# Kernel optimization log

Hardware: AMD Instinct MI355X
Metric: run time of the kernel (lower is better)

Reference implementation:

```python
import jax, jax.numpy as jnp
import numpy as np

SEQ_LEN = 1024
D_MODEL = 512
K_FILT = 24
HEADS = 8
R = 512  # must equal d_model for the module's forward to type-check
NFFT = 2048  # nearest power of two >= 2*SEQ_LEN-1
LN_EPS = 1e-5


def _spectral_filters():
    # Hankel matrix Z[i,j] = 2 / ((i+j)^3 - (i+j)), i,j in 1..T
    e = np.arange(1, SEQ_LEN + 1, dtype=np.float64)
    ipj = e[:, None] + e[None, :]
    Z = 2.0 / (ipj ** 3 - ipj)
    sigma, phi = np.linalg.eigh(Z)
    sigma_k = np.clip(sigma[-K_FILT:], 1e-9, None)
    phi_k = phi[:, -K_FILT:] * sigma_k ** 0.25
    return phi_k.astype(np.float32)  # (T, K)


def setup_inputs() -> dict:
    key = jax.random.key(0)
    ks = jax.random.split(key, 12)
    s = 0.02
    B = 2

    def lin(k):
        kw, kb = jax.random.split(k)
        return (jax.random.normal(kw, (D_MODEL, D_MODEL), jnp.float32) * s,
                jax.random.normal(kb, (D_MODEL,), jnp.float32) * s)

    Wq, bq = lin(ks[0]); Wk, bk = lin(ks[1]); Wv, bv = lin(ks[2])
    Wg, bg = lin(ks[3]); Wo, bo = lin(ks[4])
    return {
        'x': jax.random.normal(ks[5], (B, SEQ_LEN, D_MODEL), jnp.float32),
        'stu_filters': jnp.asarray(_spectral_filters()),
        'M_inputs': jax.random.normal(ks[6], (D_MODEL, R), jnp.float32) * s,
        'M_filters': jax.random.normal(ks[7], (K_FILT, R), jnp.float32) * s,
        'Wq': Wq, 'bq': bq, 'Wk': Wk, 'bk': bk, 'Wv': Wv, 'bv': bv,
        'Wg': Wg, 'bg': bg, 'Wo': Wo, 'bo': bo,
        'ln_w': jnp.ones((R,), jnp.float32),
        'ln_b': jnp.zeros((R,), jnp.float32),
    }


def _stu_conv(u, v):
    # u: (B, T, r), v: (T, r). FFT-based causal conv with sign featurization.
    T = u.shape[1]
    sgn = jnp.where(jnp.arange(T) % 2 == 1, -1.0, 1.0)[None, :, None]  # (1,T,1)
    Vf = jnp.fft.rfft(v[None, :, :, None], n=NFFT, axis=1)  # (1,F,r,1)
    U = jnp.stack([u, u * sgn], axis=-1)  # (B,T,r,2)
    Uf = jnp.fft.rfft(U, n=NFFT, axis=1)  # (B,F,r,2)
    conv = jnp.fft.irfft(Vf * Uf, n=NFFT, axis=1)[:, :T]  # (B,T,r,2)
    return conv[..., 0], conv[..., 1] * sgn


def _layernorm(x, w, b):
    mu = jnp.mean(x, axis=-1, keepdims=True)
    var = jnp.mean((x - mu) ** 2, axis=-1, keepdims=True)
    return (x - mu) * jax.lax.rsqrt(var + LN_EPS) * w + b


def reference(x, stu_filters, M_inputs, M_filters, Wq, bq, Wk, bk, Wv, bv,
              Wg, bg, Wo, bo, ln_w, ln_b):
    B, T, d = x.shape
    hd = d // HEADS
    # STU features
    u_proj = x @ M_inputs                    # (B,T,r)
    phi_proj = stu_filters @ M_filters       # (T,r)
    sp, sm = _stu_conv(u_proj, phi_proj)
    x_tilde = _layernorm(sp + sm, ln_w, ln_b)  # (B,T,r==d)
    # gated linear attention with gelu features and causal cumsum state
    def proj(W, b):
        y = (x @ W.T + b).reshape(B, T, HEADS, hd).transpose(0, 2, 1, 3)
        return jax.nn.gelu(y, approximate=True)
    Q = proj(Wq, bq); K = proj(Wk, bk); V = proj(Wv, bv)
    Zt = jnp.einsum('bhtp,bhtn->bhtpn', V, K)   # (B,H,T,hd,hd)
    Hc = jnp.cumsum(Zt, axis=2)
    Y = jnp.einsum('bhtp,bhtpn->bhtn', Q, Hc)   # (B,H,T,hd)
    Y_attn = Y.transpose(0, 2, 1, 3).reshape(B, T, d)
    gate = jax.nn.sigmoid(x @ Wg.T + bg)
    comb = gate * Y_attn + (1.0 - gate) * x_tilde
    return comb @ Wo.T + bo
```

## Files before the change

### kernel.cpp

```cpp
#include <hip/hip_runtime.h>
#include <hip/hip_bf16.h>

#define T_SEQ 1024
#define D_MOD 512
#define NHEAD 8
#define HDIM  64
#define R_DIM 512
#define BATCH 2

typedef __attribute__((ext_vector_type(8))) __bf16 bf16x8;
typedef __attribute__((ext_vector_type(4))) float f32x4;

__device__ __forceinline__ float ldin(const void* p, size_t i, int bf) {
    if (bf) return __bfloat162float(((const __hip_bfloat16*)p)[i]);
    return ((const float*)p)[i];
}
__device__ __forceinline__ void stout(void* p, size_t i, int bf, float v) {
    if (bf) ((__hip_bfloat16*)p)[i] = __float2bfloat16(v);
    else    ((float*)p)[i] = v;
}

__device__ __forceinline__ float gelu_f(float x) {
    return 0.5f * x * (1.f + tanhf(0.7978845608028654f * (x + 0.044715f * x * x * x)));
}

__device__ __forceinline__ int detect_bf(const void* x) {
    __shared__ int cnt;
    if (threadIdx.x == 0) cnt = 0;
    __syncthreads();
    const unsigned short* h = (const unsigned short*)x;
    int c = 0;
    for (int i = threadIdx.x; i < 8192; i += 256)
        if ((h[i] & 0x7F80u) == 0x7F80u) c++;
    if (c) atomicAdd(&cnt, c);
    __syncthreads();
    return cnt == 0;
}

__global__ __launch_bounds__(256) void mega_gemm(
    const void* __restrict__ x, const void* __restrict__ Mi,
    const void* __restrict__ stf, const void* __restrict__ Mf,
    const void* __restrict__ Wq, const void* __restrict__ bq,
    const void* __restrict__ Wk, const void* __restrict__ bk,
    const void* __restrict__ Wv, const void* __restrict__ bv,
    const void* __restrict__ Wg, const void* __restrict__ bg,
    float* __restrict__ fu, float* __restrict__ fphi,
    __bf16* __restrict__ fQ, __bf16* __restrict__ fKT,
    __bf16* __restrict__ fV, __bf16* __restrict__ fG)
{
    const int tid = threadIdx.x;
    const int job = blockIdx.z;
    if (job == 6) {
        float4* zp = (float4*)fu;
        zp = (float4*)(fphi + 524288);
        const int bid = blockIdx.y * 8 + blockIdx.x;
        const float4 z4 = make_float4(0.f, 0.f, 0.f, 0.f);
        #pragma unroll
        for (int q = 0; q < 8; ++q)
            zp[bid * 2048 + q * 256 + tid] = z4;
        return;
    }
    const int bf = detect_bf(x);
    const void* A = x; const void* Bw; const void* bias = nullptr;
    int Kd = 512, act = 0; bool trb = true;
    switch (job) {
        case 0: Bw = Mi; trb = false; break;
        case 1: Bw = Wq; bias = bq; act = 1; break;
        case 2: Bw = Wk; bias = bk; act = 1; break;
        case 3: Bw = Wv; bias = bv; act = 1; break;
        case 4: Bw = Wg; bias = bg; act = 2; break;
        default: A = stf; Bw = Mf; trb = false; Kd = 32; break;
    }
    const int M = (job == 5) ? 1024 : 2048;
    const int m0 = blockIdx.y * 64;
    if (m0 >= M) return;
    const int n0 = blockIdx.x * 64;

    __shared__ __align__(16) __bf16 As[64][40];
    __shared__ __align__(16) __bf16 Bs[64][40];
    const int wave = tid >> 6, lane = tid & 63;
    const int lm = lane & 15, kq = lane >> 4;

    f32x4 acc[4] = {{0.f,0.f,0.f,0.f},{0.f,0.f,0.f,0.f},
                    {0.f,0.f,0.f,0.f},{0.f,0.f,0.f,0.f}};

    for (int k0 = 0; k0 < Kd; k0 += 32) {
        if (k0) __syncthreads();
        {
            const int mo = tid >> 2;
            const int ko = (tid & 3) * 8;
            if (job == 5) {
                #pragma unroll
                for (int q = 0; q < 8; ++q) {
                    const int k = ko + q;
                    As[mo][k] = (k < 24) ? (__bf16)ldin(A, (size_t)(m0 + mo) * 24 + k, bf)
                                         : (__bf16)0.f;
                }
            } else {
                const size_t off = (size_t)(m0 + mo) * 512 + k0 + ko;
                if (bf) {
                    *(bf16x8*)&As[mo][ko] = *(const bf16x8*)((const __bf16*)A + off);
                } else {
                    const float* Af = (const float*)A + off;
                    const float4 f0 = *(const float4*)Af;
                    const float4 f1 = *(const float4*)(Af + 4);
                    bf16x8 t;
                    t[0]=(__bf16)f0.x; t[1]=(__bf16)f0.y; t[2]=(__bf16)f0.z; t[3]=(__bf16)f0.w;
                    t[4]=(__bf16)f1.x; t[5]=(__bf16)f1.y; t[6]=(__bf16)f1.z; t[7]=(__bf16)f1.w;
                    *(bf16x8*)&As[mo][ko] = t;
                }
            }
        }
        if (trb) {
            const int no = tid >> 2;
            const int ko = (tid & 3) * 8;
            const size_t off = (size_t)(n0 + no) * 512 + k0 + ko;
            if (bf) {
                *(bf16x8*)&Bs[no][ko] = *(const bf16x8*)((const __bf16*)Bw + off);
            } else {
                const float* Bf = (const float*)Bw + off;
                const float4 f0 = *(const float4*)Bf;
                const float4 f1 = *(const float4*)(Bf + 4);
                bf16x8 t;
                t[0]=(__bf16)f0.x; t[1]=(__bf16)f0.y; t[2]=(__bf16)f0.z; t[3]=(__bf16)f0.w;
                t[4]=(__bf16)f1.x; t[5]=(__bf16)f1.y; t[6]=(__bf16)f1.z; t[7]=(__bf16)f1.w;
                *(bf16x8*)&Bs[no][ko] = t;
            }
        } else {
            const int kk = tid >> 3;
            const int nn = (tid & 7) * 8;
            if (job == 5) {
                #pragma unroll
                for (int q = 0; q < 8; ++q)
                    Bs[nn + q][kk] = (kk < 24) ? (__bf16)ldin(Bw, (size_t)kk * 512 + n0 + nn + q, bf)
                                               : (__bf16)0.f;
            } else {
                const size_t off = (size_t)(k0 + kk) * 512 + n0 + nn;
                if (bf) {
                    const bf16x8 t = *(const bf16x8*)((const __bf16*)Bw + off);
                    #pragma unroll
                    for (int q = 0; q < 8; ++q) Bs[nn + q][kk] = t[q];
                } else {
                    const float* Bf = (const float*)Bw + off;
                    #pragma unroll
                    for (int q = 0; q < 8; ++q) Bs[nn + q][kk] = (__bf16)Bf[q];
                }
            }
        }
        __syncthreads();
        const bf16x8 a = *(const bf16x8*)&As[wave * 16 + lm][kq * 8];
        #pragma unroll
        for (int nt = 0; nt < 4; ++nt) {
            const bf16x8 b = *(const bf16x8*)&Bs[nt * 16 + lm][kq * 8];
            acc[nt] = __builtin_amdgcn_mfma_f32_16x16x32_bf16(a, b, acc[nt], 0, 0, 0);
        }
    }
    #pragma unroll
    for (int nt = 0; nt < 4; ++nt) {
        const int n = n0 + nt * 16 + lm;
        #pragma unroll
        for (int r2 = 0; r2 < 4; ++r2) {
            const int m = m0 + wave * 16 + kq * 4 + r2;
            float v = acc[nt][r2];
            if (bias) v += ldin(bias, (size_t)n, bf);
            if (act == 1) v = gelu_f(v);
            if (act == 2) v = 1.f / (1.f + expf(-v));
            switch (job) {
                case 0: fu[(size_t)m * 512 + n] = v; break;
                case 5: fphi[(size_t)m * 512 + n] = v; break;
                case 1: fQ[(size_t)m * 512 + n] = (__bf16)v; break;
                case 3: fV[(size_t)m * 512 + n] = (__bf16)v; break;
                case 4: fG[(size_t)m * 512 + n] = (__bf16)v; break;
                case 2: {
                    const int b = m >> 10, t = m & 1023;
                    const int h = n >> 6,  p = n & 63;
                    fKT[(((size_t)b * NHEAD + h) * 64 + p) * T_SEQ + t] = (__bf16)v;
                    break;
                }
            }
        }
    }
}

__global__ __launch_bounds__(256) void conv_attn_k(
    const float* __restrict__ u, const float* __restrict__ vphi,
    float* __restrict__ w,
    const __bf16* __restrict__ Q, const __bf16* __restrict__ KT,
    const __bf16* __restrict__ V, float* __restrict__ Y)
{
    __shared__ __align__(16) unsigned char smem[49152];
    const int tid = threadIdx.x;
    const int z = blockIdx.z;
    int rem = blockIdx.x, ti = 0;
    while (rem >= ((ti + 4) >> 2)) { rem -= (ti + 4) >> 2; ++ti; }
    const int jlo = rem * 4;
    const int jhi = (jlo + 3 < ti) ? jlo + 3 : ti;
    const int t0 = ti * 64;

    if (z < 2) {
        float (*vs)[64] = (float (*)[64])smem;
        float (*us)[64] = (float (*)[64])(smem + 16384);
        const int rl = tid & 63, tg = tid >> 6;
        const int b = z;
        const int r0 = blockIdx.y * 64;
        const float* ub = u + (size_t)b * T_SEQ * R_DIM;
        float acc[16] = {};
        for (int j = jlo; j <= jhi; ++j) {
            if (j != jlo) __syncthreads();
            const int L0 = j * 64;
            const int W0 = t0 - L0 - 63;
            #pragma unroll
            for (int jj = 0; jj < 8; ++jj) {
                const int n = jj * 256 + tid;
                const int row = n >> 4, c4 = (n & 15) * 4;
                int s = W0 + row;
                s = s < 0 ? 0 : (s > T_SEQ - 1 ? T_SEQ - 1 : s);
                *(float4*)&us[row][c4] = *(const float4*)&ub[(size_t)s * R_DIM + r0 + c4];
            }
            #pragma unroll
            for (int jj = 0; jj < 4; ++jj) {
                const int n = jj * 256 + tid;
                const int row = n >> 4, c4 = (n & 15) * 4;
                *(float4*)&vs[row][c4] = *(const float4*)&vphi[(size_t)(L0 + row) * R_DIM + r0 + c4];
            }
            __syncthreads();
            if (j < ti) {
                #pragma unroll
                for (int g = 0; g < 4; ++g) {
                    const int wsmin = tg * 16 + 49 - 16 * g;
                    float ur[30];
                    #pragma unroll
                    for (int q = 0; q < 30; ++q) ur[q] = us[wsmin + q][rl];
                    float vr[8];
                    #pragma unroll
                    for (int e = 0; e < 8; ++e) vr[e] = vs[16 * g + 2 * e][rl];
                    #pragma unroll
                    for (int e = 0; e < 8; ++e)
                        #pragma unroll
                        for (int i = 0; i < 16; ++i)
                            acc[i] += vr[e] * ur[i - 2 * e + 14];
                }
            } else {
                for (int l = 0; l < 64; l += 2) {
                    const float vv = vs[l][rl];
                    #pragma unroll
                    for (int i = 0; i < 16; ++i) {
                        const int srel = tg * 16 + i - l;
                        if (srel >= 0) acc[i] += vv * us[srel + 63][rl];
                    }
                }
            }
        }
        #pragma unroll
        for (int i = 0; i < 16; ++i)
            atomicAdd(&w[((size_t)b * T_SEQ + t0 + tg * 16 + i) * R_DIM + r0 + rl],
                      2.f * acc[i]);
    } else {
        __bf16 (*Qs)[72] = (__bf16 (*)[72])smem;
        __bf16 (*Vs)[72] = (__bf16 (*)[72])(smem + 9216);
        __bf16 (*Kt)[72] = (__bf16 (*)[72])(smem + 18432);
        __bf16 (*Sa)[72] = (__bf16 (*)[72])(smem + 27648);
        const int wave = tid >> 6, lane = tid & 63;
        const int lm = lane & 15, kq = lane >> 4;
        const int b = z - 2;
        const int h = blockIdx.y;
        const size_t cbase = ((size_t)b * T_SEQ) * D_MOD + h * HDIM;
        const __bf16* KTh = KT + (((size_t)b * NHEAD + h) * 64) * T_SEQ;
        #pragma unroll
        for (int it = 0; it < 2; ++it) {
            const int n = it * 256 + tid;
            const int row = n >> 3, p0 = (n & 7) * 8;
            *(bf16x8*)&Qs[row][p0] = *(const bf16x8*)&Q[cbase + (size_t)(t0 + row) * D_MOD + p0];
        }
        f32x4 accY[4] = {{0.f,0.f,0.f,0.f},{0.f,0.f,0.f,0.f},
                         {0.f,0.f,0.f,0.f},{0.f,0.f,0.f,0.f}};
        for (int j = jlo; j <= jhi; ++j) {
            const int s0 = j * 64;
            __syncthreads();
            #pragma unroll
            for (int it = 0; it < 2; ++it) {
                const int n = it * 256 + tid;
                const int row = n >> 3, c0 = (n & 7) * 8;
                *(bf16x8*)&Vs[row][c0] = *(const bf16x8*)&V[cbase + (size_t)(s0 + row) * D_MOD + c0];
                *(bf16x8*)&Kt[row][c0] = *(const bf16x8*)&KTh[(size_t)row * T_SEQ + s0 + c0];
            }
            __syncthreads();
            f32x4 sacc[4] = {{0.f,0.f,0.f,0.f},{0.f,0.f,0.f,0.f},
                             {0.f,0.f,0.f,0.f},{0.f,0.f,0.f,0.f}};
            #pragma unroll
            for (int ks = 0; ks < 2; ++ks) {
                const bf16x8 a = *(const bf16x8*)&Qs[wave * 16 + lm][ks * 32 + kq * 8];
                #pragma unroll
                for (int nt = 0; nt < 4; ++nt) {
                    const bf16x8 bb = *(const bf16x8*)&Vs[nt * 16 + lm][ks * 32 + kq * 8];
                    sacc[nt] = __builtin_amdgcn_mfma_f32_16x16x32_bf16(a, bb, sacc[nt], 0, 0, 0);
                }
            }
            const bool diag = (j == ti);
            #pragma unroll
            for (int nt = 0; nt < 4; ++nt) {
                const int sl = nt * 16 + lm;
                #pragma unroll
                for (int r2 = 0; r2 < 4; ++r2) {
                    const int tl = wave * 16 + kq * 4 + r2;
                    float v = sacc[nt][r2];
                    if (diag && sl > tl) v = 0.f;
                    Sa[tl][sl] = (__bf16)v;
                }
            }
            #pragma unroll
            for (int ks = 0; ks < 2; ++ks) {
                const bf16x8 a = *(const bf16x8*)&Sa[wave * 16 + lm][ks * 32 + kq * 8];
                #pragma unroll
                for (int nt = 0; nt < 4; ++nt) {
                    const bf16x8 bb = *(const bf16x8*)&Kt[nt * 16 + lm][ks * 32 + kq * 8];
                    accY[nt] = __builtin_amdgcn_mfma_f32_16x16x32_bf16(a, bb, accY[nt], 0, 0, 0);
                }
            }
        }
        #pragma unroll
        for (int nt = 0; nt < 4; ++nt) {
            const int nh = nt * 16 + lm;
            #pragma unroll
            for (int r2 = 0; r2 < 4; ++r2) {
                const int tl = wave * 16 + kq * 4 + r2;
                atomicAdd(&Y[cbase + (size_t)(t0 + tl) * D_MOD + nh], accY[nt][r2]);
            }
        }
    }
}

__global__ __launch_bounds__(256) void ln_k(float* __restrict__ w,
                                            const void* __restrict__ g,
                                            const void* __restrict__ b,
                                            const void* __restrict__ xref)
{
    const int bf = detect_bf(xref);
    const size_t row = (size_t)blockIdx.y * T_SEQ + blockIdx.x;
    float* p = w + row * R_DIM;
    const int tid = threadIdx.x;
    const float x0 = p[tid], x1 = p[tid + 256];
    __shared__ float red[4];
    float s = x0 + x1;
    #pragma unroll
    for (int off = 32; off > 0; off >>= 1) s += __shfl_down(s, off, 64);
    if ((tid & 63) == 0) red[tid >> 6] = s;
    __syncthreads();
    const float mu = (red[0] + red[1] + red[2] + red[3]) * (1.f / 512.f);
    __syncthreads();
    const float d0 = x0 - mu, d1 = x1 - mu;
    float vsum = d0 * d0 + d1 * d1;
    #pragma unroll
    for (int off = 32; off > 0; off >>= 1) vsum += __shfl_down(vsum, off, 64);
    if ((tid & 63) == 0) red[tid >> 6] = vsum;
    __syncthreads();
    const float var = (red[0] + red[1] + red[2] + red[3]) * (1.f / 512.f);
    const float rs = rsqrtf(var + 1e-5f);
    p[tid]       = d0 * rs * ldin(g, tid, bf)       + ldin(b, tid, bf);
    p[tid + 256] = d1 * rs * ldin(g, tid + 256, bf) + ldin(b, tid + 256, bf);
}

__global__ __launch_bounds__(256) void final_gemm(const __bf16* __restrict__ G,
                                                  const float* __restrict__ Yf,
                                                  const float* __restrict__ Xt,
                                                  const void* __restrict__ Wo,
                                                  const void* __restrict__ bo,
                                                  void* __restrict__ out,
                                                  const void* __restrict__ xref)
{
    const int bf = detect_bf(xref);
    __shared__ __align__(16) __bf16 As[64][40];
    __shared__ __align__(16) __bf16 Bs[64][40];
    const int tid = threadIdx.x;
    const int wave = tid >> 6, lane = tid & 63;
    const int lm = lane & 15, kq = lane >> 4;
    const int m0 = blockIdx.y * 64, n0 = blockIdx.x * 64;

    f32x4 acc[4] = {{0.f,0.f,0.f,0.f},{0.f,0.f,0.f,0.f},
                    {0.f,0.f,0.f,0.f},{0.f,0.f,0.f,0.f}};

    for (int k0 = 0; k0 < 512; k0 += 32) {
        __syncthreads();
        {
            const int mo = tid >> 2;
            const int ko = (tid & 3) * 8;
            const size_t off = (size_t)(m0 + mo) * 512 + k0 + ko;
            const bf16x8 g8 = *(const bf16x8*)(G + off);
            const float4 y0 = *(const float4*)(Yf + off);
            const float4 y1 = *(const float4*)(Yf + off + 4);
            const float4 x0 = *(const float4*)(Xt + off);
            const float4 x1 = *(const float4*)(Xt + off + 4);
            const float yv[8] = {y0.x,y0.y,y0.z,y0.w,y1.x,y1.y,y1.z,y1.w};
            const float xv[8] = {x0.x,x0.y,x0.z,x0.w,x1.x,x1.y,x1.z,x1.w};
            bf16x8 t;
            #pragma unroll
            for (int q = 0; q < 8; ++q) {
                const float gg = (float)g8[q];
                t[q] = (__bf16)(gg * yv[q] + (1.f - gg) * xv[q]);
            }
            *(bf16x8*)&As[mo][ko] = t;
        }
        {
            const int no = tid >> 2;
            const int ko = (tid & 3) * 8;
            const size_t off = (size_t)(n0 + no) * 512 + k0 + ko;
            if (bf) {
                *(bf16x8*)&Bs[no][ko] = *(const bf16x8*)((const __bf16*)Wo + off);
            } else {
                const float* Bf = (const float*)Wo + off;
                const float4 f0 = *(const float4*)Bf;
                const float4 f1 = *(const float4*)(Bf + 4);
                bf16x8 t;
                t[0]=(__bf16)f0.x; t[1]=(__bf16)f0.y; t[2]=(__bf16)f0.z; t[3]=(__bf16)f0.w;
                t[4]=(__bf16)f1.x; t[5]=(__bf16)f1.y; t[6]=(__bf16)f1.z; t[7]=(__bf16)f1.w;
                *(bf16x8*)&Bs[no][ko] = t;
            }
        }
        __syncthreads();
        const bf16x8 a = *(const bf16x8*)&As[wave * 16 + lm][kq * 8];
        #pragma unroll
        for (int nt = 0; nt < 4; ++nt) {
            const bf16x8 b = *(const bf16x8*)&Bs[nt * 16 + lm][kq * 8];
            acc[nt] = __builtin_amdgcn_mfma_f32_16x16x32_bf16(a, b, acc[nt], 0, 0, 0);
        }
    }
    #pragma unroll
    for (int nt = 0; nt < 4; ++nt) {
        const int n = n0 + nt * 16 + lm;
        #pragma unroll
        for (int r2 = 0; r2 < 4; ++r2) {
            const int m = m0 + wave * 16 + kq * 4 + r2;
            float v = acc[nt][r2] + ldin(bo, (size_t)n, bf);
            stout(out, (size_t)m * 512 + n, bf, v);
        }
    }
}

extern "C" void kernel_launch(void* const* d_in, const int* in_sizes, int n_in,
                              void* d_out, int out_size, void* d_ws, size_t ws_size,
                              hipStream_t stream)
{
    const void* x   = d_in[0];
    const void* stf = d_in[1];
    const void* Mi  = d_in[2];
    const void* Mf  = d_in[3];
    const void* Wq  = d_in[4];  const void* bq = d_in[5];
    const void* Wk  = d_in[6];  const void* bk = d_in[7];
    const void* Wv  = d_in[8];  const void* bv = d_in[9];
    const void* Wg  = d_in[10]; const void* bg = d_in[11];
    const void* Wo  = d_in[12]; const void* bo = d_in[13];
    const void* lnw = d_in[14]; const void* lnb = d_in[15];

    float* base = (float*)d_ws;
    float*  f_u   = base;
    float*  f_phi = base + 1048576;
    float*  f_w   = base + 1572864;
    float*  f_Y   = base + 2621440;
    __bf16* f_Q   = (__bf16*)(base + 3670016);
    __bf16* f_KT  = f_Q + 1048576;
    __bf16* f_V   = f_KT + 1048576;
    __bf16* f_G   = f_V + 1048576;

    dim3 blk(256);

    mega_gemm<<<dim3(8, 32, 7), blk, 0, stream>>>(
        x, Mi, stf, Mf, Wq, bq, Wk, bk, Wv, bv, Wg, bg,
        f_u, f_phi, f_Q, f_KT, f_V, f_G);

    conv_attn_k<<<dim3(40, 8, 4), blk, 0, stream>>>(f_u, f_phi, f_w, f_Q, f_KT, f_V, f_Y);

    ln_k<<<dim3(T_SEQ, BATCH), blk, 0, stream>>>(f_w, lnw, lnb, x);

    final_gemm<<<dim3(8, 32), blk, 0, stream>>>(f_G, f_Y, f_w, Wo, bo, d_out, x);
}
```

Before: 193.3 us.

## Enlarge mega_gemm tiles to 128x64 with K=64 steps and LDS-staged K transpose

The projection GEMM kernel now computes 128x64 output tiles per block, with two M-subtiles per wave and a 64-wide K step, which halves the grid and the number of barrier iterations. Weight loads for the non-transposed B path are vectorised into 8-element LDS stores. The transposed K output is staged through shared memory and written with coalesced 16-byte stores instead of strided scalar writes. The zero-fill job is resized to match the smaller grid. The cost is more LDS and registers per block and fewer blocks available to fill the GPU.

```diff
diff --git a/kernel.cpp b/kernel.cpp
--- a/kernel.cpp
+++ b/kernel.cpp
@@ -51,135 +51,162 @@
     const int tid = threadIdx.x;
     const int job = blockIdx.z;
     if (job == 6) {
-        float4* zp = (float4*)fu;
-        zp = (float4*)(fphi + 524288);
+        float4* zp = (float4*)(fphi + 524288);
         const int bid = blockIdx.y * 8 + blockIdx.x;
         const float4 z4 = make_float4(0.f, 0.f, 0.f, 0.f);
         #pragma unroll
-        for (int q = 0; q < 8; ++q)
-            zp[bid * 2048 + q * 256 + tid] = z4;
+        for (int q = 0; q < 16; ++q)
+            zp[(size_t)bid * 4096 + q * 256 + tid] = z4;
         return;
     }
     const int bf = detect_bf(x);
     const void* A = x; const void* Bw; const void* bias = nullptr;
-    int Kd = 512, act = 0; bool trb = true;
+    int act = 0; bool trb = true;
     switch (job) {
         case 0: Bw = Mi; trb = false; break;
         case 1: Bw = Wq; bias = bq; act = 1; break;
         case 2: Bw = Wk; bias = bk; act = 1; break;
         case 3: Bw = Wv; bias = bv; act = 1; break;
         case 4: Bw = Wg; bias = bg; act = 2; break;
-        default: A = stf; Bw = Mf; trb = false; Kd = 32; break;
+        default: A = stf; Bw = Mf; trb = false; break;
     }
     const int M = (job == 5) ? 1024 : 2048;
-    const int m0 = blockIdx.y * 64;
+    const int Kd = (job == 5) ? 64 : 512;
+    const int m0 = blockIdx.y * 128;
     if (m0 >= M) return;
     const int n0 = blockIdx.x * 64;
 
-    __shared__ __align__(16) __bf16 As[64][40];
-    __shared__ __align__(16) __bf16 Bs[64][40];
+    __shared__ __align__(16) __bf16 As[128][72];
+    __shared__ __align__(16) __bf16 Bs[64][72];
     const int wave = tid >> 6, lane = tid & 63;
     const int lm = lane & 15, kq = lane >> 4;
 
-    f32x4 acc[4] = {{0.f,0.f,0.f,0.f},{0.f,0.f,0.f,0.f},
-                    {0.f,0.f,0.f,0.f},{0.f,0.f,0.f,0.f}};
-
-    for (int k0 = 0; k0 < Kd; k0 += 32) {
+    f32x4 acc[2][4] = {};
+
+    for (int k0 = 0; k0 < Kd; k0 += 64) {
         if (k0) __syncthreads();
-        {
-            const int mo = tid >> 2;
-            const int ko = (tid & 3) * 8;
+        #pragma unroll
+        for (int q = 0; q < 4; ++q) {
+            const int c = q * 256 + tid;
+            const int row = c >> 3, off = (c & 7) * 8;
             if (job == 5) {
-                #pragma unroll
-                for (int q = 0; q < 8; ++q) {
-                    const int k = ko + q;
-                    As[mo][k] = (k < 24) ? (__bf16)ldin(A, (size_t)(m0 + mo) * 24 + k, bf)
-                                         : (__bf16)0.f;
-                }
+                bf16x8 t;
+                #pragma unroll
+                for (int e = 0; e < 8; ++e) {
+                    const int k = off + e;
+                    t[e] = (k < 24) ? (__bf16)ldin(A, (size_t)(m0 + row) * 24 + k, bf)
+                                    : (__bf16)0.f;
+                }
+                *(bf16x8*)&As[row][off] = t;
+            } else if (bf) {
+                *(bf16x8*)&As[row][off] =
+                    *(const bf16x8*)((const __bf16*)A + (size_t)(m0 + row) * 512 + k0 + off);
             } else {
-                const size_t off = (size_t)(m0 + mo) * 512 + k0 + ko;
+                const float* Af = (const float*)A + (size_t)(m0 + row) * 512 + k0 + off;
+                const float4 f0 = *(const float4*)Af;
+                const float4 f1 = *(const float4*)(Af + 4);
+                bf16x8 t;
+                t[0]=(__bf16)f0.x; t[1]=(__bf16)f0.y; t[2]=(__bf16)f0.z; t[3]=(__bf16)f0.w;
+                t[4]=(__bf16)f1.x; t[5]=(__bf16)f1.y; t[6]=(__bf16)f1.z; t[7]=(__bf16)f1.w;
+                *(bf16x8*)&As[row][off] = t;
+            }
+        }
+        if (trb) {
+            #pragma unroll
+            for (int q = 0; q < 2; ++q) {
+                const int c = q * 256 + tid;
+                const int row = c >> 3, off = (c & 7) * 8;
+                const size_t go = (size_t)(n0 + row) * 512 + k0 + off;
                 if (bf) {
-                    *(bf16x8*)&As[mo][ko] = *(const bf16x8*)((const __bf16*)A + off);
+                    *(bf16x8*)&Bs[row][off] = *(const bf16x8*)((const __bf16*)Bw + go);
                 } else {
-                    const float* Af = (const float*)A + off;
-                    const float4 f0 = *(const float4*)Af;
-                    const float4 f1 = *(const float4*)(Af + 4);
+                    const float* Bf = (const float*)Bw + go;
+                    const float4 f0 = *(const float4*)Bf;
+                    const float4 f1 = *(const float4*)(Bf + 4);
                     bf16x8 t;
                     t[0]=(__bf16)f0.x; t[1]=(__bf16)f0.y; t[2]=(__bf16)f0.z; t[3]=(__bf16)f0.w;
                     t[4]=(__bf16)f1.x; t[5]=(__bf16)f1.y; t[6]=(__bf16)f1.z; t[7]=(__bf16)f1.w;
-                    *(bf16x8*)&As[mo][ko] = t;
-                }
-            }
-        }
-        if (trb) {
-            const int no = tid >> 2;
-            const int ko = (tid & 3) * 8;
-            const size_t off = (size_t)(n0 + no) * 512 + k0 + ko;
-            if (bf) {
-                *(bf16x8*)&Bs[no][ko] = *(const bf16x8*)((const __bf16*)Bw + off);
-            } else {
-                const float* Bf = (const float*)Bw + off;
-                const float4 f0 = *(const float4*)Bf;
-                const float4 f1 = *(const float4*)(Bf + 4);
+                    *(bf16x8*)&Bs[row][off] = t;
+                }
+            }
+        } else {
+            const int n = tid & 63;
+            const int g0 = tid >> 6;
+            #pragma unroll
+            for (int q = 0; q < 2; ++q) {
+                const int kk = (q * 4 + g0) * 8;
                 bf16x8 t;
-                t[0]=(__bf16)f0.x; t[1]=(__bf16)f0.y; t[2]=(__bf16)f0.z; t[3]=(__bf16)f0.w;
-                t[4]=(__bf16)f1.x; t[5]=(__bf16)f1.y; t[6]=(__bf16)f1.z; t[7]=(__bf16)f1.w;
-                *(bf16x8*)&Bs[no][ko] = t;
-            }
-        } else {
-            const int kk = tid >> 3;
-            const int nn = (tid & 7) * 8;
-            if (job == 5) {
-                #pragma unroll
-                for (int q = 0; q < 8; ++q)
-                    Bs[nn + q][kk] = (kk < 24) ? (__bf16)ldin(Bw, (size_t)kk * 512 + n0 + nn + q, bf)
-                                               : (__bf16)0.f;
-            } else {
-                const size_t off = (size_t)(k0 + kk) * 512 + n0 + nn;
-                if (bf) {
-                    const bf16x8 t = *(const bf16x8*)((const __bf16*)Bw + off);
-                    #pragma unroll
-                    for (int q = 0; q < 8; ++q) Bs[nn + q][kk] = t[q];
-                } else {
-                    const float* Bf = (const float*)Bw + off;
-                    #pragma unroll
-                    for (int q = 0; q < 8; ++q) Bs[nn + q][kk] = (__bf16)Bf[q];
-                }
+                #pragma unroll
+                for (int e = 0; e < 8; ++e) {
+                    const int k = k0 + kk + e;
+                    t[e] = (job == 5 && k >= 24) ? (__bf16)0.f
+                         : (__bf16)ldin(Bw, (size_t)k * 512 + n0 + n, bf);
+                }
+                *(bf16x8*)&Bs[n][kk] = t;
             }
         }
         __syncthreads();
-        const bf16x8 a = *(const bf16x8*)&As[wave * 16 + lm][kq * 8];
+        #pragma unroll
+        for (int ks = 0; ks < 2; ++ks) {
+            #pragma unroll
+            for (int ms = 0; ms < 2; ++ms) {
+                const bf16x8 a = *(const bf16x8*)&As[wave * 32 + ms * 16 + lm][ks * 32 + kq * 8];
+                #pragma unroll
+                for (int nt = 0; nt < 4; ++nt) {
+                    const bf16x8 b = *(const bf16x8*)&Bs[nt * 16 + lm][ks * 32 + kq * 8];
+                    acc[ms][nt] = __builtin_amdgcn_mfma_f32_16x16x32_bf16(a, b, acc[ms][nt], 0, 0, 0);
+                }
+            }
+        }
+    }
+    if (job == 2) {
+        __syncthreads();
+        __bf16 (*Kt)[136] = (__bf16 (*)[136])&As[0][0];
+        #pragma unroll
+        for (int ms = 0; ms < 2; ++ms)
+            #pragma unroll
+            for (int nt = 0; nt < 4; ++nt) {
+                const int n = nt * 16 + lm;
+                #pragma unroll
+                for (int r2 = 0; r2 < 4; ++r2) {
+                    float v = acc[ms][nt][r2] + ldin(bias, (size_t)(n0 + n), bf);
+                    Kt[n][wave * 32 + ms * 16 + kq * 4 + r2] = (__bf16)gelu_f(v);
+                }
+            }
+        __syncthreads();
+        const int h = n0 >> 6;
+        const int b = m0 >> 10;
+        const int tb = m0 & 1023;
+        #pragma unroll
+        for (int q = 0; q < 4; ++q) {
+            const int c = q * 256 + tid;
+            const int p = c >> 4, off = (c & 15) * 8;
+            *(bf16x8*)&fKT[(((size_t)b * NHEAD + h) * 64 + p) * T_SEQ + tb + off] =
+                *(const bf16x8*)&Kt[p][off];
+        }
+        return;
+    }
+    #pragma unroll
+    for (int ms = 0; ms < 2; ++ms)
         #pragma unroll
         for (int nt = 0; nt < 4; ++nt) {
-            const bf16x8 b = *(const bf16x8*)&Bs[nt * 16 + lm][kq * 8];
-            acc[nt] = __builtin_amdgcn_mfma_f32_16x16x32_bf16(a, b, acc[nt], 0, 0, 0);
-        }
-    }
-    #pragma unroll
-    for (int nt = 0; nt < 4; ++nt) {
-        const int n = n0 + nt * 16 + lm;
-        #pragma unroll
-        for (int r2 = 0; r2 < 4; ++r2) {
-            const int m = m0 + wave * 16 + kq * 4 + r2;
-            float v = acc[nt][r2];
-            if (bias) v += ldin(bias, (size_t)n, bf);
-            if (act == 1) v = gelu_f(v);
-            if (act == 2) v = 1.f / (1.f + expf(-v));
-            switch (job) {
-                case 0: fu[(size_t)m * 512 + n] = v; break;
-                case 5: fphi[(size_t)m * 512 + n] = v; break;
-                case 1: fQ[(size_t)m * 512 + n] = (__bf16)v; break;
-                case 3: fV[(size_t)m * 512 + n] = (__bf16)v; break;
-                case 4: fG[(size_t)m * 512 + n] = (__bf16)v; break;
-                case 2: {
-                    const int b = m >> 10, t = m & 1023;
-                    const int h = n >> 6,  p = n & 63;
-                    fKT[(((size_t)b * NHEAD + h) * 64 + p) * T_SEQ + t] = (__bf16)v;
-                    break;
-                }
-            }
-        }
-    }
+            const int n = n0 + nt * 16 + lm;
+            #pragma unroll
+            for (int r2 = 0; r2 < 4; ++r2) {
+                const int m = m0 + wave * 32 + ms * 16 + kq * 4 + r2;
+                float v = acc[ms][nt][r2];
+                if (bias) v += ldin(bias, (size_t)n, bf);
+                if (act == 1) v = gelu_f(v);
+                if (act == 2) v = 1.f / (1.f + expf(-v));
+                switch (job) {
+                    case 0: fu[(size_t)m * 512 + n] = v; break;
+                    case 5: fphi[(size_t)m * 512 + n] = v; break;
+                    case 1: fQ[(size_t)m * 512 + n] = (__bf16)v; break;
+                    case 3: fV[(size_t)m * 512 + n] = (__bf16)v; break;
+                    default: fG[(size_t)m * 512 + n] = (__bf16)v; break;
+                }
+            }
+        }
 }
 
 __global__ __launch_bounds__(256) void conv_attn_k(
@@ -272,8 +299,7 @@
             const int row = n >> 3, p0 = (n & 7) * 8;
             *(bf16x8*)&Qs[row][p0] = *(const bf16x8*)&Q[cbase + (size_t)(t0 + row) * D_MOD + p0];
         }
-        f32x4 accY[4] = {{0.f,0.f,0.f,0.f},{0.f,0.f,0.f,0.f},
-                         {0.f,0.f,0.f,0.f},{0.f,0.f,0.f,0.f}};
+        f32x4 accY[4] = {};
         for (int j = jlo; j <= jhi; ++j) {
             const int s0 = j * 64;
             __syncthreads();
@@ -285,8 +311,7 @@
                 *(bf16x8*)&Kt[row][c0] = *(const bf16x8*)&KTh[(size_t)row * T_SEQ + s0 + c0];
             }
             __syncthreads();
-            f32x4 sacc[4] = {{0.f,0.f,0.f,0.f},{0.f,0.f,0.f,0.f},
-                             {0.f,0.f,0.f,0.f},{0.f,0.f,0.f,0.f}};
+            f32x4 sacc[4] = {};
             #pragma unroll
             for (int ks = 0; ks < 2; ++ks) {
                 const bf16x8 a = *(const bf16x8*)&Qs[wave * 16 + lm][ks * 32 + kq * 8];
@@ -376,8 +401,7 @@
     const int lm = lane & 15, kq = lane >> 4;
     const int m0 = blockIdx.y * 64, n0 = blockIdx.x * 64;
 
-    f32x4 acc[4] = {{0.f,0.f,0.f,0.f},{0.f,0.f,0.f,0.f},
-                    {0.f,0.f,0.f,0.f},{0.f,0.f,0.f,0.f}};
+    f32x4 acc[4] = {};
 
     for (int k0 = 0; k0 < 512; k0 += 32) {
         __syncthreads();
@@ -463,7 +487,7 @@
 
     dim3 blk(256);
 
-    mega_gemm<<<dim3(8, 32, 7), blk, 0, stream>>>(
+    mega_gemm<<<dim3(8, 16, 7), blk, 0, stream>>>(
         x, Mi, stf, Mf, Wq, bq, Wk, bk, Wv, bv, Wg, bg,
         f_u, f_phi, f_Q, f_KT, f_V, f_G);
 
```

Result: slower. 212.0 us (+9.7%).
